# Optimization experiments

Measured on AMD Instinct MI355X. Metric: run time of the kernel, lower is better.

The kernel has to match this reference:

```python
import jax, jax.numpy as jnp
import numpy as np

MODEL_DIM = 256
PAIR_IMPORTANCE_WEIGHT = 0.5
B, S, D = 4, 4096, MODEL_DIM


def setup_inputs() -> dict:
    key = jax.random.key(0)
    ks = jax.random.split(key, 6)
    return {
        "query": jax.random.normal(ks[0], (B, S, D), dtype=jnp.float32),
        "key": jax.random.normal(ks[1], (B, S, D), dtype=jnp.float32),
        "value": jax.random.normal(ks[2], (B, S, D), dtype=jnp.float32),
        "W_query": jax.random.normal(ks[3], (D, D), dtype=jnp.float32),
        "W_key": jax.random.normal(ks[4], (D, D), dtype=jnp.float32),
        "W_value": jax.random.normal(ks[5], (D, D), dtype=jnp.float32),
    }


def reference(query, key, value, W_query, W_key, W_value):
    # Projections: [B,S,D] @ [D,D]
    q = jnp.einsum('bsd,de->bse', query, W_query)
    k = jnp.einsum('bsd,de->bse', key, W_key)
    v = jnp.einsum('bsd,de->bse', value, W_value)
    scale = jnp.sqrt(jnp.asarray(MODEL_DIM, dtype=q.dtype))
    # Full [B,S,S] score matrix (global max forces materialization)
    scores = jnp.einsum('bqd,bkd->bqk', q, k) / scale
    s_len = scores.shape[1]
    diag_bias = jnp.eye(s_len, dtype=scores.dtype) * jnp.max(scores)
    scores = scores + PAIR_IMPORTANCE_WEIGHT * diag_bias  # broadcast over batch
    attention_weights = jax.nn.softmax(scores, axis=-1)
    output = jnp.einsum('bqk,bkd->bqd', attention_weights, v)
    return output, attention_weights
```

## Files before the change

### kernel.cpp

```cpp
#include <hip/hip_runtime.h>
#include <cstdint>
#include <cstddef>

#define BB 4
#define SS 4096
#define DD 256
#define SCORE_SCALE (1.0f/16.0f)
#define PIW 0.5f
#define NROWS (BB * SS)

typedef float          f32x4  __attribute__((ext_vector_type(4)));
typedef __bf16         bf16v8 __attribute__((ext_vector_type(8)));
typedef unsigned short u16v8  __attribute__((ext_vector_type(8)));
typedef unsigned short u16v4  __attribute__((ext_vector_type(4)));

__device__ __forceinline__ f32x4 mfma_bf16(u16v8 a, u16v8 b, f32x4 c) {
    return __builtin_amdgcn_mfma_f32_16x16x32_bf16(
        __builtin_bit_cast(bf16v8, a), __builtin_bit_cast(bf16v8, b), c, 0, 0, 0);
}

__device__ __forceinline__ unsigned short f2bf(float f) {
    unsigned u = __float_as_uint(f);
    u += 0x7FFFu + ((u >> 16) & 1u);
    return (unsigned short)(u >> 16);
}
__device__ __forceinline__ float bf2f(unsigned short h) {
    return __uint_as_float(((unsigned)h) << 16);
}
__device__ __forceinline__ unsigned fenc(float x) {
    unsigned u = __float_as_uint(x);
    return (u & 0x80000000u) ? ~u : (u | 0x80000000u);
}
__device__ __forceinline__ float fdec(unsigned e) {
    return __uint_as_float((e & 0x80000000u) ? (e ^ 0x80000000u) : ~e);
}

#define TM 128
#define TN 128
#define TK 16
#define PADW 132

__global__ __launch_bounds__(256) void proj_kernel(
    const float* __restrict__ query, const float* __restrict__ key_, const float* __restrict__ value,
    const float* __restrict__ Wq, const float* __restrict__ Wk, const float* __restrict__ Wv,
    unsigned short* __restrict__ qh, unsigned short* __restrict__ ql,
    unsigned short* __restrict__ kh, unsigned short* __restrict__ kl,
    unsigned short* __restrict__ vT, unsigned* __restrict__ gmax)
{
    const int z = blockIdx.z;
    const float* A = (z == 0) ? query : (z == 1) ? key_ : value;
    const float* W = (z == 0) ? Wq    : (z == 1) ? Wk   : Wv;
    if (z == 0 && blockIdx.x == 0 && blockIdx.y == 0 && threadIdx.x == 0)
        *gmax = 0x007FFFFFu;

    const int K = DD, N = DD;
    __shared__ float As[TK][PADW];
    __shared__ float Bs[TK][PADW];
    const int tid = threadIdx.x;
    const int tx = tid & 15, ty = tid >> 4;
    const int rowBase = blockIdx.y * TM;
    const int colBase = blockIdx.x * TN;

    float acc[8][8] = {};

    for (int k0 = 0; k0 < K; k0 += TK) {
        #pragma unroll
        for (int i = 0; i < 2; i++) {
            int idx = tid + i * 256;
            int r = idx >> 2, kq = idx & 3;
            const float4 av = *(const float4*)&A[(size_t)(rowBase + r) * K + k0 + kq * 4];
            As[kq * 4 + 0][r] = av.x; As[kq * 4 + 1][r] = av.y;
            As[kq * 4 + 2][r] = av.z; As[kq * 4 + 3][r] = av.w;
        }
        #pragma unroll
        for (int i = 0; i < 2; i++) {
            int idx = tid + i * 256;
            int kk = idx >> 5, cq = idx & 31;
            *(float4*)&Bs[kk][cq * 4] = *(const float4*)&W[(size_t)(k0 + kk) * N + colBase + cq * 4];
        }
        __syncthreads();
        #pragma unroll
        for (int kk = 0; kk < TK; kk++) {
            float a[8], b[8];
            *(float4*)&a[0] = *(const float4*)&As[kk][ty * 8];
            *(float4*)&a[4] = *(const float4*)&As[kk][ty * 8 + 4];
            *(float4*)&b[0] = *(const float4*)&Bs[kk][tx * 8];
            *(float4*)&b[4] = *(const float4*)&Bs[kk][tx * 8 + 4];
            #pragma unroll
            for (int i = 0; i < 8; i++)
                #pragma unroll
                for (int j = 0; j < 8; j++)
                    acc[i][j] = fmaf(a[i], b[j], acc[i][j]);
        }
        __syncthreads();
    }

    #pragma unroll
    for (int i = 0; i < 8; i++) {
        const int gr = rowBase + ty * 8 + i;
        if (z == 2) {
            const int b2 = gr >> 12, s2 = gr & (SS - 1);
            #pragma unroll
            for (int j = 0; j < 8; j++) {
                int col = colBase + tx * 8 + j;
                vT[((size_t)b2 * DD + col) * SS + s2] = f2bf(acc[i][j]);
            }
        } else {
            unsigned short h[8], l[8];
            #pragma unroll
            for (int j = 0; j < 8; j++) {
                h[j] = f2bf(acc[i][j]);
                l[j] = f2bf(acc[i][j] - bf2f(h[j]));
            }
            unsigned short* H = (z == 0) ? qh : kh;
            unsigned short* L = (z == 0) ? ql : kl;
            size_t base = (size_t)gr * DD + colBase + tx * 8;
            *(u16v4*)&H[base]     = (u16v4){h[0], h[1], h[2], h[3]};
            *(u16v4*)&H[base + 4] = (u16v4){h[4], h[5], h[6], h[7]};
            *(u16v4*)&L[base]     = (u16v4){l[0], l[1], l[2], l[3]};
            *(u16v4*)&L[base + 4] = (u16v4){l[4], l[5], l[6], l[7]};
        }
    }
}

#define SPAD 40

__global__ __launch_bounds__(256) void scores_mfma(
    const unsigned short* __restrict__ qh, const unsigned short* __restrict__ ql,
    const unsigned short* __restrict__ kh, const unsigned short* __restrict__ kl,
    float* __restrict__ attn, unsigned* __restrict__ gmax,
    float* __restrict__ tmaxg, float* __restrict__ tsumg)
{
    const int b = blockIdx.z;
    const size_t boff = (size_t)b * SS * DD;
    const unsigned short* Qh = qh + boff;
    const unsigned short* Ql = ql + boff;
    const unsigned short* Kh = kh + boff;
    const unsigned short* Kl = kl + boff;
    float* C = attn + (size_t)b * SS * SS;

    __shared__ unsigned short Ah[128][SPAD];
    __shared__ unsigned short Al[128][SPAD];
    __shared__ unsigned short Bh[128][SPAD];
    __shared__ unsigned short Bl[128][SPAD];
    __shared__ float s_m[4][64];
    __shared__ float s_s[4][64];
    __shared__ float red[128];

    const int tid = threadIdx.x;
    const int lane = tid & 63, w = tid >> 6;
    const int wr = (w >> 1) * 64, wc = (w & 1) * 64;
    const int m = lane & 15, qq = lane >> 4;
    const int rowBase = blockIdx.y * 128;
    const int colBase = blockIdx.x * 128;

    f32x4 acc[4][4];
    #pragma unroll
    for (int i = 0; i < 4; i++)
        #pragma unroll
        for (int j = 0; j < 4; j++)
            acc[i][j] = (f32x4){0.f, 0.f, 0.f, 0.f};

    const int chunk = (tid & 3) * 8;
    const int srow  = tid >> 2;

    for (int k0 = 0; k0 < DD; k0 += 32) {
        #pragma unroll
        for (int i = 0; i < 2; i++) {
            int r = srow + i * 64;
            size_t ga = (size_t)(rowBase + r) * DD + k0 + chunk;
            size_t gb = (size_t)(colBase + r) * DD + k0 + chunk;
            *(u16v8*)&Ah[r][chunk] = *(const u16v8*)&Qh[ga];
            *(u16v8*)&Al[r][chunk] = *(const u16v8*)&Ql[ga];
            *(u16v8*)&Bh[r][chunk] = *(const u16v8*)&Kh[gb];
            *(u16v8*)&Bl[r][chunk] = *(const u16v8*)&Kl[gb];
        }
        __syncthreads();

        const int kb = qq * 8;
        u16v8 ah[4], al[4], bh[4], bl[4];
        #pragma unroll
        for (int i = 0; i < 4; i++) {
            ah[i] = *(const u16v8*)&Ah[wr + i * 16 + m][kb];
            al[i] = *(const u16v8*)&Al[wr + i * 16 + m][kb];
            bh[i] = *(const u16v8*)&Bh[wc + i * 16 + m][kb];
            bl[i] = *(const u16v8*)&Bl[wc + i * 16 + m][kb];
        }
        #pragma unroll
        for (int i = 0; i < 4; i++)
            #pragma unroll
            for (int j = 0; j < 4; j++) {
                acc[i][j] = mfma_bf16(ah[i], bh[j], acc[i][j]);
                acc[i][j] = mfma_bf16(ah[i], bl[j], acc[i][j]);
                acc[i][j] = mfma_bf16(al[i], bh[j], acc[i][j]);
            }
        __syncthreads();
    }

    #pragma unroll
    for (int i = 0; i < 4; i++)
        #pragma unroll
        for (int j = 0; j < 4; j++)
            acc[i][j] *= SCORE_SCALE;

    #pragma unroll
    for (int i = 0; i < 4; i++)
        #pragma unroll
        for (int j = 0; j < 4; j++)
            #pragma unroll
            for (int r = 0; r < 4; r++) {
                int row = rowBase + wr + i * 16 + qq * 4 + r;
                int col = colBase + wc + j * 16 + m;
                __builtin_nontemporal_store(acc[i][j][r], &C[(size_t)row * SS + col]);
            }

    float lmax[16];
    #pragma unroll
    for (int i = 0; i < 4; i++)
        #pragma unroll
        for (int r = 0; r < 4; r++)
            lmax[i * 4 + r] = fmaxf(fmaxf(acc[i][0][r], acc[i][1][r]),
                                    fmaxf(acc[i][2][r], acc[i][3][r]));
    #pragma unroll
    for (int t = 0; t < 16; t++) {
        #pragma unroll
        for (int msk = 1; msk < 16; msk <<= 1)
            lmax[t] = fmaxf(lmax[t], __shfl_xor(lmax[t], msk));
    }
    if (m == 0) {
        #pragma unroll
        for (int i = 0; i < 4; i++)
            #pragma unroll
            for (int r = 0; r < 4; r++)
                s_m[w][i * 16 + qq * 4 + r] = lmax[i * 4 + r];
    }
    __syncthreads();
    float lsum[16];
    #pragma unroll
    for (int i = 0; i < 4; i++)
        #pragma unroll
        for (int r = 0; r < 4; r++) {
            int idx = i * 16 + qq * 4 + r;
            float rm = fmaxf(s_m[w][idx], s_m[w ^ 1][idx]);
            float s = 0.f;
            #pragma unroll
            for (int j = 0; j < 4; j++)
                s += __expf(acc[i][j][r] - rm);
            lsum[i * 4 + r] = s;
        }
    #pragma unroll
    for (int t = 0; t < 16; t++) {
        #pragma unroll
        for (int msk = 1; msk < 16; msk <<= 1)
            lsum[t] += __shfl_xor(lsum[t], msk);
    }
    if (m == 0) {
        #pragma unroll
        for (int i = 0; i < 4; i++)
            #pragma unroll
            for (int r = 0; r < 4; r++)
                s_s[w][i * 16 + qq * 4 + r] = lsum[i * 4 + r];
    }
    __syncthreads();

    if (tid < 128) {
        int wp = tid >> 6, lr = tid & 63;
        float tm = fmaxf(s_m[2 * wp][lr], s_m[2 * wp + 1][lr]);
        float ts = s_s[2 * wp][lr] + s_s[2 * wp + 1][lr];
        size_t gi = (size_t)blockIdx.x * NROWS + (size_t)b * SS + rowBase + tid;
        tmaxg[gi] = tm;
        tsumg[gi] = ts;
        red[tid] = tm;
    }
    __syncthreads();
    for (int s2 = 64; s2 > 0; s2 >>= 1) {
        if (tid < s2) red[tid] = fmaxf(red[tid], red[tid + s2]);
        __syncthreads();
    }
    if (tid == 0) atomicMax(gmax, fenc(red[0]));
}

__global__ __launch_bounds__(256) void stats_merge(
    const float* __restrict__ tmaxg, const float* __restrict__ tsumg,
    const float* __restrict__ attn, const unsigned* __restrict__ gmax,
    float* __restrict__ rowm, float* __restrict__ rowinv)
{
    const int grow = blockIdx.x * 256 + threadIdx.x;
    const int b = grow >> 12, i = grow & (SS - 1);
    const float bias = PIW * fdec(*gmax);

    float tm[32];
    float mx = -INFINITY;
    #pragma unroll
    for (int t = 0; t < 32; t++) {
        tm[t] = tmaxg[(size_t)t * NROWS + grow];
        mx = fmaxf(mx, tm[t]);
    }
    const float dii = attn[(size_t)b * SS * SS + (size_t)i * SS + i];
    mx = fmaxf(mx, dii + bias);

    float s = 0.f;
    #pragma unroll
    for (int t = 0; t < 32; t++)
        s += tsumg[(size_t)t * NROWS + grow] * __expf(tm[t] - mx);
    s += __expf(dii + bias - mx) - __expf(dii - mx);

    rowm[grow] = mx;
    rowinv[grow] = 1.0f / s;
}

__global__ __launch_bounds__(256) void av_softmax_mfma(
    float* __restrict__ attn, const unsigned short* __restrict__ vT,
    const float* __restrict__ rowm, const float* __restrict__ rowinv,
    const unsigned* __restrict__ gmax, float* __restrict__ out)
{
    const int lin = blockIdx.x;
    const int b = (lin & 7) >> 1;
    const int rowTile = ((lin >> 3) << 1) | (lin & 1);
    const int rowBase = rowTile * 32;

    float* A = attn + (size_t)b * SS * SS;
    const unsigned short* Bv = vT + (size_t)b * DD * SS;
    const float bias = PIW * fdec(*gmax);

    __shared__ unsigned short As[2][32][136];

    const int tid = threadIdx.x;
    const int lane = tid & 63, w = tid >> 6;
    const int m = lane & 15, qq = lane >> 4;

    const int ra = tid >> 3;
    const int c0 = (tid & 7) * 4;
    const int rr = rowBase + ra;
    float* Arow = A + (size_t)rr * SS;
    const float mr = rowm[b * SS + rr];
    const float ri = rowinv[b * SS + rr];

    const unsigned short* Bp[4];
    #pragma unroll
    for (int j = 0; j < 4; j++)
        Bp[j] = Bv + (size_t)(w * 64 + j * 16 + m) * SS;

    f32x4 acc[2][4];
    #pragma unroll
    for (int i = 0; i < 2; i++)
        #pragma unroll
        for (int j = 0; j < 4; j++)
            acc[i][j] = (f32x4){0.f, 0.f, 0.f, 0.f};

    f32x4 pf[4];

    auto loadA = [&](int kbase) {
        #pragma unroll
        for (int u = 0; u < 4; u++)
            pf[u] = __builtin_nontemporal_load(
                (const f32x4*)&Arow[kbase + c0 + u * 32]);
    };
    auto procStore = [&](int kbase, int buf) {
        #pragma unroll
        for (int u = 0; u < 4; u++) {
            int c = c0 + u * 32;
            int j0 = kbase + c;
            float e0 = pf[u][0] + ((j0 + 0 == rr) ? bias : 0.0f);
            float e1 = pf[u][1] + ((j0 + 1 == rr) ? bias : 0.0f);
            float e2 = pf[u][2] + ((j0 + 2 == rr) ? bias : 0.0f);
            float e3 = pf[u][3] + ((j0 + 3 == rr) ? bias : 0.0f);
            float w0 = __expf(e0 - mr) * ri;
            float w1 = __expf(e1 - mr) * ri;
            float w2 = __expf(e2 - mr) * ri;
            float w3 = __expf(e3 - mr) * ri;
            f32x4 wv = (f32x4){w0, w1, w2, w3};
            __builtin_nontemporal_store(wv, (f32x4*)&Arow[j0]);
            *(u16v4*)&As[buf][ra][c] =
                (u16v4){f2bf(w0), f2bf(w1), f2bf(w2), f2bf(w3)};
        }
    };

    const int NT = SS / 128;

    loadA(0);
    procStore(0, 0);
    __syncthreads();

    for (int t = 0; t < NT; t++) {
        const int k0 = t * 128;
        const int cur = t & 1;
        if (t + 1 < NT)
            loadA(k0 + 128);
        #pragma unroll
        for (int kk = 0; kk < 4; kk++) {
            const int kb = kk * 32 + qq * 8;
            u16v8 bf_[4], af_[2];
            #pragma unroll
            for (int j = 0; j < 4; j++)
                bf_[j] = *(const u16v8*)&Bp[j][k0 + kb];
            #pragma unroll
            for (int i = 0; i < 2; i++)
                af_[i] = *(const u16v8*)&As[cur][i * 16 + m][kb];
            #pragma unroll
            for (int i = 0; i < 2; i++)
                #pragma unroll
                for (int j = 0; j < 4; j++)
                    acc[i][j] = mfma_bf16(af_[i], bf_[j], acc[i][j]);
        }
        if (t + 1 < NT) {
            procStore(k0 + 128, cur ^ 1);
            __syncthreads();
        }
    }

    #pragma unroll
    for (int i = 0; i < 2; i++) {
        #pragma unroll
        for (int j = 0; j < 4; j++) {
            #pragma unroll
            for (int r = 0; r < 4; r++) {
                int row = rowBase + i * 16 + qq * 4 + r;
                int col = w * 64 + j * 16 + m;
                __builtin_nontemporal_store(
                    acc[i][j][r], &out[((size_t)b * SS + row) * DD + col]);
            }
        }
    }
}

extern "C" void kernel_launch(void* const* d_in, const int* in_sizes, int n_in,
                              void* d_out, int out_size, void* d_ws, size_t ws_size,
                              hipStream_t stream)
{
    const float* query = (const float*)d_in[0];
    const float* key_  = (const float*)d_in[1];
    const float* value = (const float*)d_in[2];
    const float* Wq    = (const float*)d_in[3];
    const float* Wk    = (const float*)d_in[4];
    const float* Wv    = (const float*)d_in[5];

    float* out  = (float*)d_out;
    float* attn = out + (size_t)BB * SS * DD;

    const size_t E = (size_t)BB * SS * DD;
    unsigned short* qh = (unsigned short*)d_ws;
    unsigned short* ql = qh + E;
    unsigned short* kh = ql + E;
    unsigned short* kl = kh + E;
    unsigned short* vT = kl + E;
    float* tmaxg  = (float*)(vT + E);
    float* tsumg  = tmaxg + 32 * (size_t)NROWS;
    float* rowm   = tsumg + 32 * (size_t)NROWS;
    float* rowinv = rowm + NROWS;
    unsigned* gmax = (unsigned*)(rowinv + NROWS);

    proj_kernel<<<dim3(DD / TN, (BB * SS) / TM, 3), 256, 0, stream>>>(
        query, key_, value, Wq, Wk, Wv, qh, ql, kh, kl, vT, gmax);
    scores_mfma<<<dim3(SS / 128, SS / 128, BB), 256, 0, stream>>>(
        qh, ql, kh, kl, attn, gmax, tmaxg, tsumg);
    stats_merge<<<dim3(NROWS / 256), 256, 0, stream>>>(
        tmaxg, tsumg, attn, gmax, rowm, rowinv);
    av_softmax_mfma<<<dim3(512), 256, 0, stream>>>(
        attn, vT, rowm, rowinv, gmax, out);
}
```

Before: 672.7 us.

## Use split-bf16 MFMA projection and halve AV row tile with deeper prefetch

The fp32 FMA projection GEMM is replaced by an MFMA version. Inputs and weights are split into bf16 hi/lo parts and three products are accumulated to keep near-fp32 accuracy. Separately, the softmax+AV kernel drops from 32-row to 16-row tiles, doubling the grid to 1024 blocks, and prefetches the attention rows two tiles ahead. This aims to cut projection compute time and raise parallelism and latency hiding in the bandwidth-bound AV pass, at the cost of scalar uncoalesced stores in the projection epilogue and twice the vT reads per output row.

```diff
diff --git a/kernel.cpp b/kernel.cpp
--- a/kernel.cpp
+++ b/kernel.cpp
@@ -35,10 +35,7 @@
     return __uint_as_float((e & 0x80000000u) ? (e ^ 0x80000000u) : ~e);
 }
 
-#define TM 128
-#define TN 128
-#define TK 16
-#define PADW 132
+#define PSPAD 42
 
 __global__ __launch_bounds__(256) void proj_kernel(
     const float* __restrict__ query, const float* __restrict__ key_, const float* __restrict__ value,
@@ -53,72 +50,102 @@
     if (z == 0 && blockIdx.x == 0 && blockIdx.y == 0 && threadIdx.x == 0)
         *gmax = 0x007FFFFFu;
 
-    const int K = DD, N = DD;
-    __shared__ float As[TK][PADW];
-    __shared__ float Bs[TK][PADW];
+    __shared__ unsigned short Ah[128][PSPAD];
+    __shared__ unsigned short Al[128][PSPAD];
+    __shared__ unsigned short Bh[128][PSPAD];
+    __shared__ unsigned short Bl[128][PSPAD];
+
     const int tid = threadIdx.x;
-    const int tx = tid & 15, ty = tid >> 4;
-    const int rowBase = blockIdx.y * TM;
-    const int colBase = blockIdx.x * TN;
-
-    float acc[8][8] = {};
-
-    for (int k0 = 0; k0 < K; k0 += TK) {
+    const int lane = tid & 63, w = tid >> 6;
+    const int wr = (w >> 1) * 64, wc = (w & 1) * 64;
+    const int m = lane & 15, qq = lane >> 4;
+    const int rowBase = blockIdx.y * 128;
+    const int colBase = blockIdx.x * 128;
+
+    f32x4 acc[4][4];
+    #pragma unroll
+    for (int i = 0; i < 4; i++)
+        #pragma unroll
+        for (int j = 0; j < 4; j++)
+            acc[i][j] = (f32x4){0.f, 0.f, 0.f, 0.f};
+
+    const int chunk = (tid & 3) * 8;
+    const int srow  = tid >> 2;
+
+    for (int k0 = 0; k0 < DD; k0 += 32) {
         #pragma unroll
         for (int i = 0; i < 2; i++) {
+            int r = srow + i * 64;
+            const float* src = &A[(size_t)(rowBase + r) * DD + k0 + chunk];
+            float4 f0 = *(const float4*)src;
+            float4 f1 = *(const float4*)(src + 4);
+            float v[8] = {f0.x, f0.y, f0.z, f0.w, f1.x, f1.y, f1.z, f1.w};
+            u16v8 h, l;
+            #pragma unroll
+            for (int e = 0; e < 8; e++) {
+                h[e] = f2bf(v[e]);
+                l[e] = f2bf(v[e] - bf2f(h[e]));
+            }
+            *(u16v8*)&Ah[r][chunk] = h;
+            *(u16v8*)&Al[r][chunk] = l;
+        }
+        #pragma unroll
+        for (int i = 0; i < 4; i++) {
             int idx = tid + i * 256;
-            int r = idx >> 2, kq = idx & 3;
-            const float4 av = *(const float4*)&A[(size_t)(rowBase + r) * K + k0 + kq * 4];
-            As[kq * 4 + 0][r] = av.x; As[kq * 4 + 1][r] = av.y;
-            As[kq * 4 + 2][r] = av.z; As[kq * 4 + 3][r] = av.w;
-        }
-        #pragma unroll
-        for (int i = 0; i < 2; i++) {
-            int idx = tid + i * 256;
-            int kk = idx >> 5, cq = idx & 31;
-            *(float4*)&Bs[kk][cq * 4] = *(const float4*)&W[(size_t)(k0 + kk) * N + colBase + cq * 4];
+            int kk = idx >> 5, nq = idx & 31;
+            float4 f = *(const float4*)&W[(size_t)(k0 + kk) * DD + colBase + nq * 4];
+            float v[4] = {f.x, f.y, f.z, f.w};
+            #pragma unroll
+            for (int e = 0; e < 4; e++) {
+                unsigned short h = f2bf(v[e]);
+                unsigned short l = f2bf(v[e] - bf2f(h));
+                Bh[nq * 4 + e][kk] = h;
+                Bl[nq * 4 + e][kk] = l;
+            }
         }
         __syncthreads();
-        #pragma unroll
-        for (int kk = 0; kk < TK; kk++) {
-            float a[8], b[8];
-            *(float4*)&a[0] = *(const float4*)&As[kk][ty * 8];
-            *(float4*)&a[4] = *(const float4*)&As[kk][ty * 8 + 4];
-            *(float4*)&b[0] = *(const float4*)&Bs[kk][tx * 8];
-            *(float4*)&b[4] = *(const float4*)&Bs[kk][tx * 8 + 4];
-            #pragma unroll
-            for (int i = 0; i < 8; i++)
-                #pragma unroll
-                for (int j = 0; j < 8; j++)
-                    acc[i][j] = fmaf(a[i], b[j], acc[i][j]);
-        }
+
+        const int kb = qq * 8;
+        u16v8 ah[4], al[4], bh[4], bl[4];
+        #pragma unroll
+        for (int i = 0; i < 4; i++) {
+            ah[i] = *(const u16v8*)&Ah[wr + i * 16 + m][kb];
+            al[i] = *(const u16v8*)&Al[wr + i * 16 + m][kb];
+            bh[i] = *(const u16v8*)&Bh[wc + i * 16 + m][kb];
+            bl[i] = *(const u16v8*)&Bl[wc + i * 16 + m][kb];
+        }
+        #pragma unroll
+        for (int i = 0; i < 4; i++)
+            #pragma unroll
+            for (int j = 0; j < 4; j++) {
+                acc[i][j] = mfma_bf16(ah[i], bh[j], acc[i][j]);
+                acc[i][j] = mfma_bf16(ah[i], bl[j], acc[i][j]);
+                acc[i][j] = mfma_bf16(al[i], bh[j], acc[i][j]);
+            }
         __syncthreads();
     }
 
     #pragma unroll
-    for (int i = 0; i < 8; i++) {
-        const int gr = rowBase + ty * 8 + i;
-        if (z == 2) {
-            const int b2 = gr >> 12, s2 = gr & (SS - 1);
-            #pragma unroll
-            for (int j = 0; j < 8; j++) {
-                int col = colBase + tx * 8 + j;
-                vT[((size_t)b2 * DD + col) * SS + s2] = f2bf(acc[i][j]);
-            }
-        } else {
-            unsigned short h[8], l[8];
-            #pragma unroll
-            for (int j = 0; j < 8; j++) {
-                h[j] = f2bf(acc[i][j]);
-                l[j] = f2bf(acc[i][j] - bf2f(h[j]));
-            }
-            unsigned short* H = (z == 0) ? qh : kh;
-            unsigned short* L = (z == 0) ? ql : kl;
-            size_t base = (size_t)gr * DD + colBase + tx * 8;
-            *(u16v4*)&H[base]     = (u16v4){h[0], h[1], h[2], h[3]};
-            *(u16v4*)&H[base + 4] = (u16v4){h[4], h[5], h[6], h[7]};
-            *(u16v4*)&L[base]     = (u16v4){l[0], l[1], l[2], l[3]};
-            *(u16v4*)&L[base + 4] = (u16v4){l[4], l[5], l[6], l[7]};
+    for (int i = 0; i < 4; i++) {
+        #pragma unroll
+        for (int j = 0; j < 4; j++) {
+            #pragma unroll
+            for (int r = 0; r < 4; r++) {
+                const int gr  = rowBase + wr + i * 16 + qq * 4 + r;
+                const int col = colBase + wc + j * 16 + m;
+                const float v = acc[i][j][r];
+                if (z == 2) {
+                    const int b2 = gr >> 12, s2 = gr & (SS - 1);
+                    vT[((size_t)b2 * DD + col) * SS + s2] = f2bf(v);
+                } else {
+                    unsigned short h = f2bf(v);
+                    unsigned short l = f2bf(v - bf2f(h));
+                    unsigned short* H = (z == 0) ? qh : kh;
+                    unsigned short* L = (z == 0) ? ql : kl;
+                    H[(size_t)gr * DD + col] = h;
+                    L[(size_t)gr * DD + col] = l;
+                }
+            }
         }
     }
 }
@@ -317,20 +344,20 @@
     const int lin = blockIdx.x;
     const int b = (lin & 7) >> 1;
     const int rowTile = ((lin >> 3) << 1) | (lin & 1);
-    const int rowBase = rowTile * 32;
+    const int rowBase = rowTile * 16;
 
     float* A = attn + (size_t)b * SS * SS;
     const unsigned short* Bv = vT + (size_t)b * DD * SS;
     const float bias = PIW * fdec(*gmax);
 
-    __shared__ unsigned short As[2][32][136];
+    __shared__ unsigned short As[2][16][136];
 
     const int tid = threadIdx.x;
     const int lane = tid & 63, w = tid >> 6;
     const int m = lane & 15, qq = lane >> 4;
 
-    const int ra = tid >> 3;
-    const int c0 = (tid & 7) * 4;
+    const int ra = tid >> 4;
+    const int ch = tid & 15;
     const int rr = rowBase + ra;
     float* Arow = A + (size_t)rr * SS;
     const float mr = rowm[b * SS + rr];
@@ -341,30 +368,28 @@
     for (int j = 0; j < 4; j++)
         Bp[j] = Bv + (size_t)(w * 64 + j * 16 + m) * SS;
 
-    f32x4 acc[2][4];
-    #pragma unroll
-    for (int i = 0; i < 2; i++)
-        #pragma unroll
-        for (int j = 0; j < 4; j++)
-            acc[i][j] = (f32x4){0.f, 0.f, 0.f, 0.f};
-
-    f32x4 pf[4];
-
-    auto loadA = [&](int kbase) {
-        #pragma unroll
-        for (int u = 0; u < 4; u++)
-            pf[u] = __builtin_nontemporal_load(
-                (const f32x4*)&Arow[kbase + c0 + u * 32]);
+    f32x4 acc[4];
+    #pragma unroll
+    for (int j = 0; j < 4; j++)
+        acc[j] = (f32x4){0.f, 0.f, 0.f, 0.f};
+
+    f32x4 pfs[2][2];
+
+    auto loadA = [&](int kbase, int slot) {
+        #pragma unroll
+        for (int u = 0; u < 2; u++)
+            pfs[slot][u] = __builtin_nontemporal_load(
+                (const f32x4*)&Arow[kbase + ch * 4 + u * 64]);
     };
-    auto procStore = [&](int kbase, int buf) {
-        #pragma unroll
-        for (int u = 0; u < 4; u++) {
-            int c = c0 + u * 32;
+    auto procStore = [&](int kbase, int slot, int buf) {
+        #pragma unroll
+        for (int u = 0; u < 2; u++) {
+            int c = ch * 4 + u * 64;
             int j0 = kbase + c;
-            float e0 = pf[u][0] + ((j0 + 0 == rr) ? bias : 0.0f);
-            float e1 = pf[u][1] + ((j0 + 1 == rr) ? bias : 0.0f);
-            float e2 = pf[u][2] + ((j0 + 2 == rr) ? bias : 0.0f);
-            float e3 = pf[u][3] + ((j0 + 3 == rr) ? bias : 0.0f);
+            float e0 = pfs[slot][u][0] + ((j0 + 0 == rr) ? bias : 0.0f);
+            float e1 = pfs[slot][u][1] + ((j0 + 1 == rr) ? bias : 0.0f);
+            float e2 = pfs[slot][u][2] + ((j0 + 2 == rr) ? bias : 0.0f);
+            float e3 = pfs[slot][u][3] + ((j0 + 3 == rr) ? bias : 0.0f);
             float w0 = __expf(e0 - mr) * ri;
             float w1 = __expf(e1 - mr) * ri;
             float w2 = __expf(e2 - mr) * ri;
@@ -378,48 +403,42 @@
 
     const int NT = SS / 128;
 
-    loadA(0);
-    procStore(0, 0);
+    loadA(0, 0);
+    procStore(0, 0, 0);
+    loadA(128, 1);
     __syncthreads();
 
     for (int t = 0; t < NT; t++) {
         const int k0 = t * 128;
         const int cur = t & 1;
-        if (t + 1 < NT)
-            loadA(k0 + 128);
+        if (t + 2 < NT)
+            loadA(k0 + 256, cur);
         #pragma unroll
         for (int kk = 0; kk < 4; kk++) {
             const int kb = kk * 32 + qq * 8;
-            u16v8 bf_[4], af_[2];
+            u16v8 bf_[4];
             #pragma unroll
             for (int j = 0; j < 4; j++)
                 bf_[j] = *(const u16v8*)&Bp[j][k0 + kb];
-            #pragma unroll
-            for (int i = 0; i < 2; i++)
-                af_[i] = *(const u16v8*)&As[cur][i * 16 + m][kb];
-            #pragma unroll
-            for (int i = 0; i < 2; i++)
-                #pragma unroll
-                for (int j = 0; j < 4; j++)
-                    acc[i][j] = mfma_bf16(af_[i], bf_[j], acc[i][j]);
+            u16v8 af_ = *(const u16v8*)&As[cur][m][kb];
+            #pragma unroll
+            for (int j = 0; j < 4; j++)
+                acc[j] = mfma_bf16(af_, bf_[j], acc[j]);
         }
         if (t + 1 < NT) {
-            procStore(k0 + 128, cur ^ 1);
+            procStore(k0 + 128, (t + 1) & 1, cur ^ 1);
             __syncthreads();
         }
     }
 
     #pragma unroll
-    for (int i = 0; i < 2; i++) {
-        #pragma unroll
-        for (int j = 0; j < 4; j++) {
-            #pragma unroll
-            for (int r = 0; r < 4; r++) {
-                int row = rowBase + i * 16 + qq * 4 + r;
-                int col = w * 64 + j * 16 + m;
-                __builtin_nontemporal_store(
-                    acc[i][j][r], &out[((size_t)b * SS + row) * DD + col]);
-            }
+    for (int j = 0; j < 4; j++) {
+        #pragma unroll
+        for (int r = 0; r < 4; r++) {
+            int row = rowBase + qq * 4 + r;
+            int col = w * 64 + j * 16 + m;
+            __builtin_nontemporal_store(
+                acc[j][r], &out[((size_t)b * SS + row) * DD + col]);
         }
     }
 }
@@ -450,12 +469,12 @@
     float* rowinv = rowm + NROWS;
     unsigned* gmax = (unsigned*)(rowinv + NROWS);
 
-    proj_kernel<<<dim3(DD / TN, (BB * SS) / TM, 3), 256, 0, stream>>>(
+    proj_kernel<<<dim3(DD / 128, (BB * SS) / 128, 3), 256, 0, stream>>>(
         query, key_, value, Wq, Wk, Wv, qh, ql, kh, kl, vT, gmax);
     scores_mfma<<<dim3(SS / 128, SS / 128, BB), 256, 0, stream>>>(
         qh, ql, kh, kl, attn, gmax, tmaxg, tsumg);
     stats_merge<<<dim3(NROWS / 256), 256, 0, stream>>>(
         tmaxg, tsumg, attn, gmax, rowm, rowinv);
-    av_softmax_mfma<<<dim3(512), 256, 0, stream>>>(
+    av_softmax_mfma<<<dim3(1024), 256, 0, stream>>>(
         attn, vT, rowm, rowinv, gmax, out);
 }
```

Measured after the change: 769.6 us. 14.4% more time.
